# Performance work log

Hardware: AMD Instinct MI355X
Metric: run time of the kernel (lower is better)

The kernel has to match this reference:

```python
import jax, jax.numpy as jnp
import numpy as np

D = 4      # number of tensor modes (leaves of the HT tree)
N = 8      # input dim per mode  (total input  = 8^4 = 4096)
M = 8      # output dim per mode (total output = 8^4 = 4096)
R = 8      # HT rank
B = 512    # batch size
# preorder index of each internal-node core in the stacked `cores` array
CORE_IDX = {(0, 4): 0, (0, 2): 1, (2, 4): 2}


def _contract(a, a_names, b, b_names):
    """tn.contract_between equivalent: contract all shared named axes."""
    shared = [n for n in a_names if n in b_names]
    ax_a = [a_names.index(n) for n in shared]
    ax_b = [b_names.index(n) for n in shared]
    out = jnp.tensordot(a, b, axes=(ax_a, ax_b))
    names = [n for n in a_names if n not in shared] + [n for n in b_names if n not in shared]
    return out, names


def _fwd(x, names, lo, hi, factors, cores):
    """Faithful translation of HTSubTree.forward / build_network.

    Leaf p: factor (in_p, out_p, parent). Internal (lo,hi): core
    (left=parent(lo,mid), right=parent(mid,hi), parent=parent(lo,hi)).
    Contraction order: left subtree, then core, then right subtree; shared
    (pre-connected) edges are contracted automatically, exactly as in
    tn.contract_between on the pre-wired network.
    """
    if hi - lo == 1:
        p = lo
        f_names = [f"in_{p}", f"out_{p}", f"pr_{p}_{p + 1}"]
        return _contract(x, names, factors[p], f_names)
    mid = (lo + hi) // 2
    x, names = _fwd(x, names, lo, mid, factors, cores)
    c_names = [f"pr_{lo}_{mid}", f"pr_{mid}_{hi}", f"pr_{lo}_{hi}"]
    x, names = _contract(x, names, cores[CORE_IDX[(lo, hi)]], c_names)
    return _fwd(x, names, mid, hi, factors, cores)


def setup_inputs() -> dict:
    key = jax.random.key(0)
    k1, k2, k3 = jax.random.split(key, 3)
    x = jax.random.normal(k1, (B, N, N, N, N), dtype=jnp.float32)
    # xavier_normal(fan_in=[in], fan_out=[out, rank]) for factors
    std_f = (2.0 / (N + M * R)) ** 0.5
    factors = jax.random.normal(k2, (D, N, M, R), dtype=jnp.float32) * std_f
    # cores: xavier over rank axes
    std_c = (2.0 / (R + R * R)) ** 0.5
    cores = jax.random.normal(k3, (D - 1, R, R, R), dtype=jnp.float32) * std_c
    return {"x": x, "factors": factors, "cores": cores}


def reference(x, factors, cores):
    names = ["batch"] + [f"in_{p}" for p in range(D)]
    out, names = _fwd(x, names, 0, D, factors, cores)
    # dangling edges: batch, out_0..out_{D-1}, root parent rank -> canonical order
    order = ["batch"] + [f"out_{p}" for p in range(D)] + [f"pr_0_{D}"]
    perm = [names.index(n) for n in order]
    return jnp.transpose(out, perm)  # (B, m0, m1, m2, m3, R)
```

## Files before the change

### kernel.cpp

```cpp
#include <hip/hip_runtime.h>

typedef __attribute__((ext_vector_type(8))) short bf16x8;
typedef __attribute__((ext_vector_type(4))) float f32x4;

static __device__ __forceinline__ short f2bf(float f) {
    union { float f; unsigned u; } v; v.f = f;
    unsigned r = v.u + 0x7fffu + ((v.u >> 16) & 1u);
    return (short)(r >> 16);
}

__global__ __launch_bounds__(256) void ht_pre(const float* __restrict__ factors,
                                              const float* __restrict__ cores,
                                              short* __restrict__ TLTF,
                                              short* __restrict__ VTF) {
    const int bid = blockIdx.x, t = threadIdx.x;
    if (bid < 64) {
        __shared__ float TRl[64][9];
        const int m23 = bid;
        const int m2 = m23 >> 3, m3 = m23 & 7;
        {
            const int v = t * 2;
            const int n23 = v >> 3;
            const int r24 = v & 7;
            const int n2 = n23 >> 3, n3 = n23 & 7;
            const float* f2p = factors + 1024 + n2 * 64 + m2 * 8;
            const float* f3p = factors + 1536 + n3 * 64 + m3 * 8;
            const float* c2p = cores + 1024;
            float s0 = 0.f, s1 = 0.f;
            #pragma unroll
            for (int r23 = 0; r23 < 8; ++r23) {
                float a = f2p[r23];
                #pragma unroll
                for (int r34 = 0; r34 < 8; ++r34) {
                    float wv = a * f3p[r34];
                    s0 += wv * c2p[r23 * 64 + r34 * 8 + r24];
                    s1 += wv * c2p[r23 * 64 + r34 * 8 + r24 + 1];
                }
            }
            TRl[n23][r24] = s0;
            TRl[n23][r24 + 1] = s1;
        }
        __syncthreads();
        {
            const int r = t >> 5, seg = t & 31;
            const int k2b = seg * 16;
            const int r02 = k2b >> 6;
            float c0v[8];
            #pragma unroll
            for (int r24 = 0; r24 < 8; ++r24)
                c0v[r24] = cores[r02 * 64 + r24 * 8 + r];
            short ov[16];
            #pragma unroll
            for (int j = 0; j < 16; ++j) {
                const int n23 = (k2b + j) & 63;
                float s = 0.f;
                #pragma unroll
                for (int r24 = 0; r24 < 8; ++r24)
                    s += TRl[n23][r24] * c0v[r24];
                ov[j] = f2bf(s);
            }
            const int c = m23 * 8 + r;
            const int ct16 = c >> 4, lrow = c & 15;
            const int kb = k2b >> 5;
            const int hi0 = (k2b >> 3) & 3;
            const int base = (ct16 * 16 + kb) * 512 + lrow * 8;
            *(bf16x8*)&VTF[base + hi0 * 128]       = *(bf16x8*)&ov[0];
            *(bf16x8*)&VTF[base + (hi0 + 1) * 128] = *(bf16x8*)&ov[8];
        }
    } else {
        const int idx = ((bid - 64) * 256 + t) * 2;
        const int p = idx >> 6, n01 = idx & 63;
        const int n0 = n01 >> 3, n1 = n01 & 7;
        const int mm = p >> 3, r02 = p & 7;
        const int m0 = mm >> 3, m1 = mm & 7;
        const float* f0 = factors + n0 * 64 + m0 * 8;
        const float* f1a = factors + 512 + n1 * 64 + m1 * 8;
        const float* f1b = f1a + 64;
        const float* c1 = cores + 512;
        float s0 = 0.f, s1 = 0.f;
        #pragma unroll
        for (int r01 = 0; r01 < 8; ++r01) {
            float a = f0[r01];
            #pragma unroll
            for (int r12 = 0; r12 < 8; ++r12) {
                float cv = c1[r01 * 64 + r12 * 8 + r02];
                s0 += a * f1a[r12] * cv;
                s1 += a * f1b[r12] * cv;
            }
        }
        unsigned w0 = (unsigned short)f2bf(s0);
        unsigned w1 = (unsigned short)f2bf(s1);
        const int p16 = p >> 4, prow = p & 15;
        const int half = n01 >> 5, hi = (n01 >> 3) & 3, e = n01 & 7;
        *(unsigned*)&TLTF[(p16 * 2 + half) * 512 + (hi * 16 + prow) * 8 + e] = w0 | (w1 << 16);
    }
}

__global__ __launch_bounds__(256, 2) void ht_main(const float* __restrict__ x,
                                                  const short* __restrict__ TLTF,
                                                  const short* __restrict__ VTF,
                                                  float* __restrict__ out) {
    __shared__ short XT[64 * 64];
    __shared__ short YF[64 * 512];

    const int t = threadIdx.x;
    const int b = blockIdx.x;
    const int w = t >> 6, l = t & 63;
    const int lr = l & 15, lk = l >> 4;

    {
        const float* xb = x + b * 4096;
        #pragma unroll
        for (int j = 0; j < 4; ++j) {
            f32x4 v = *(const f32x4*)(xb + j * 1024 + t * 4);
            int n01 = j * 16 + (t >> 4);
            int rbase = (t & 15) * 4;
            #pragma unroll
            for (int e = 0; e < 4; ++e) {
                int rr = rbase + e;
                XT[rr * 64 + (n01 ^ ((rr & 7) << 3))] = f2bf(v[e]);
            }
        }
    }
    __syncthreads();

    {
        bf16x8 bx[4][2];
        #pragma unroll
        for (int ct = 0; ct < 4; ++ct) {
            int rr = ct * 16 + lr;
            #pragma unroll
            for (int kh = 0; kh < 2; ++kh)
                bx[ct][kh] = *(const bf16x8*)&XT[rr * 64 + (((kh * 4 + lk) ^ (rr & 7))) * 8];
        }
        #pragma unroll
        for (int pt = 0; pt < 8; ++pt) {
            const short* ap = TLTF + (w * 8 + pt) * 1024 + l * 8;
            bf16x8 a0 = *(const bf16x8*)ap;
            bf16x8 a1 = *(const bf16x8*)(ap + 512);
            #pragma unroll
            for (int ct = 0; ct < 4; ++ct) {
                f32x4 d = {0.f, 0.f, 0.f, 0.f};
                d = __builtin_amdgcn_mfma_f32_16x16x32_bf16(a0, bx[ct][0], d, 0, 0, 0);
                d = __builtin_amdgcn_mfma_f32_16x16x32_bf16(a1, bx[ct][1], d, 0, 0, 0);
                #pragma unroll
                for (int reg = 0; reg < 4; ++reg) {
                    int pl = lk * 4 + reg;
                    int m_lo = pt * 2 + (pl >> 3);
                    int k2 = (pl & 7) * 64 + ct * 16 + lr;
                    int kb = k2 >> 5, hi = (k2 >> 3) & 3, e = k2 & 7;
                    YF[(w * 16 + kb) * 512 + (hi * 16 + m_lo) * 8 + e] = f2bf(d[reg]);
                }
            }
        }
    }
    __syncthreads();

    {
        f32x4 acc[4][8];
        #pragma unroll
        for (int rt = 0; rt < 4; ++rt)
            #pragma unroll
            for (int ctl = 0; ctl < 8; ++ctl)
                acc[rt][ctl] = (f32x4){0.f, 0.f, 0.f, 0.f};

        bf16x8 afA[4], afB[4], bvA[8], bvB[8];

        #define LDA(kb, af_)  { _Pragma("unroll") \
            for (int rt = 0; rt < 4; ++rt) \
                af_[rt] = *(const bf16x8*)&YF[(rt * 16 + (kb)) * 512 + l * 8]; }
        #define LDB(kb, bv_)  { _Pragma("unroll") \
            for (int ctl = 0; ctl < 8; ++ctl) \
                bv_[ctl] = *(const bf16x8*)&VTF[((w * 8 + ctl) * 16 + (kb)) * 512 + l * 8]; }
        #define MM(af_, bv_)  { _Pragma("unroll") \
            for (int rt = 0; rt < 4; ++rt) { _Pragma("unroll") \
                for (int ctl = 0; ctl < 8; ++ctl) \
                    acc[rt][ctl] = __builtin_amdgcn_mfma_f32_16x16x32_bf16(af_[rt], bv_[ctl], acc[rt][ctl], 0, 0, 0); } }

        LDA(0, afA); LDB(0, bvA);
        #pragma unroll
        for (int kp = 0; kp < 8; ++kp) {
            LDA(kp * 2 + 1, afB); LDB(kp * 2 + 1, bvB);
            MM(afA, bvA);
            if (kp < 7) { LDA(kp * 2 + 2, afA); LDB(kp * 2 + 2, bvA); }
            MM(afB, bvB);
        }
        #undef LDA
        #undef LDB
        #undef MM

        float* ob = out + b * 32768 + w * 128;
        #pragma unroll
        for (int rt = 0; rt < 4; ++rt)
            #pragma unroll
            for (int ctl = 0; ctl < 8; ++ctl)
                #pragma unroll
                for (int reg = 0; reg < 4; ++reg)
                    ob[(rt * 16 + lk * 4 + reg) * 512 + ctl * 16 + lr] = acc[rt][ctl][reg];
    }
}

extern "C" void kernel_launch(void* const* d_in, const int* in_sizes, int n_in,
                              void* d_out, int out_size, void* d_ws, size_t ws_size,
                              hipStream_t stream) {
    const float* x       = (const float*)d_in[0];
    const float* factors = (const float*)d_in[1];
    const float* cores   = (const float*)d_in[2];
    float* out = (float*)d_out;

    short* TLTF = (short*)d_ws;
    short* VTF  = TLTF + 32768;

    hipLaunchKernelGGL(ht_pre, dim3(128), dim3(256), 0, stream, factors, cores, TLTF, VTF);
    hipLaunchKernelGGL(ht_main, dim3(512), dim3(256), 0, stream, x, TLTF, VTF, out);
}
```

Measured before the change: 125.9 us.

## Use 8 waves per block with swizzled row-major intermediate LDS layout

Doubles ht_main to 512 threads, so each wave owns half as many output column tiles and half the P-rows in stage one. The intermediate Y is now stored row-major in LDS with an XOR swizzle and packed 8-byte writes, replacing the scattered 2-byte stores. The VTF k-ordering in ht_pre changes to match. The explicit double-buffered load pipeline in the main GEMM is dropped in favour of a simple per-kb loop. This trades fewer registers per thread and more parallelism for the loss of manual prefetch.

```diff
diff --git a/kernel.cpp b/kernel.cpp
--- a/kernel.cpp
+++ b/kernel.cpp
@@ -2,6 +2,8 @@
 
 typedef __attribute__((ext_vector_type(8))) short bf16x8;
 typedef __attribute__((ext_vector_type(4))) float f32x4;
+
+struct u32x2 { unsigned x, y; };
 
 static __device__ __forceinline__ short f2bf(float f) {
     union { float f; unsigned u; } v; v.f = f;
@@ -43,26 +45,21 @@
         __syncthreads();
         {
             const int r = t >> 5, seg = t & 31;
-            const int k2b = seg * 16;
-            const int r02 = k2b >> 6;
-            float c0v[8];
-            #pragma unroll
-            for (int r24 = 0; r24 < 8; ++r24)
-                c0v[r24] = cores[r02 * 64 + r24 * 8 + r];
             short ov[16];
             #pragma unroll
             for (int j = 0; j < 16; ++j) {
-                const int n23 = (k2b + j) & 63;
+                const int n23 = seg * 2 + (j >> 3);
+                const int r02 = j & 7;
                 float s = 0.f;
                 #pragma unroll
                 for (int r24 = 0; r24 < 8; ++r24)
-                    s += TRl[n23][r24] * c0v[r24];
+                    s += TRl[n23][r24] * cores[r02 * 64 + r24 * 8 + r];
                 ov[j] = f2bf(s);
             }
             const int c = m23 * 8 + r;
             const int ct16 = c >> 4, lrow = c & 15;
-            const int kb = k2b >> 5;
-            const int hi0 = (k2b >> 3) & 3;
+            const int kb = seg >> 1;
+            const int hi0 = (seg * 2) & 3;
             const int base = (ct16 * 16 + kb) * 512 + lrow * 8;
             *(bf16x8*)&VTF[base + hi0 * 128]       = *(bf16x8*)&ov[0];
             *(bf16x8*)&VTF[base + (hi0 + 1) * 128] = *(bf16x8*)&ov[8];
@@ -96,12 +93,12 @@
     }
 }
 
-__global__ __launch_bounds__(256, 2) void ht_main(const float* __restrict__ x,
+__global__ __launch_bounds__(512, 2) void ht_main(const float* __restrict__ x,
                                                   const short* __restrict__ TLTF,
                                                   const short* __restrict__ VTF,
                                                   float* __restrict__ out) {
     __shared__ short XT[64 * 64];
-    __shared__ short YF[64 * 512];
+    __shared__ short YS[64 * 512];
 
     const int t = threadIdx.x;
     const int b = blockIdx.x;
@@ -111,9 +108,9 @@
     {
         const float* xb = x + b * 4096;
         #pragma unroll
-        for (int j = 0; j < 4; ++j) {
-            f32x4 v = *(const f32x4*)(xb + j * 1024 + t * 4);
-            int n01 = j * 16 + (t >> 4);
+        for (int j = 0; j < 2; ++j) {
+            f32x4 v = *(const f32x4*)(xb + j * 2048 + t * 4);
+            int n01 = j * 32 + (t >> 4);
             int rbase = (t & 15) * 4;
             #pragma unroll
             for (int e = 0; e < 4; ++e) {
@@ -131,69 +128,61 @@
             int rr = ct * 16 + lr;
             #pragma unroll
             for (int kh = 0; kh < 2; ++kh)
-                bx[ct][kh] = *(const bf16x8*)&XT[rr * 64 + (((kh * 4 + lk) ^ (rr & 7))) * 8];
-        }
-        #pragma unroll
-        for (int pt = 0; pt < 8; ++pt) {
-            const short* ap = TLTF + (w * 8 + pt) * 1024 + l * 8;
+                bx[ct][kh] = *(const bf16x8*)&XT[rr * 64 + ((kh * 4 + lk) ^ (rr & 7)) * 8];
+        }
+        #pragma unroll
+        for (int pt = 0; pt < 4; ++pt) {
+            const short* ap = TLTF + (w * 4 + pt) * 1024 + l * 8;
             bf16x8 a0 = *(const bf16x8*)ap;
             bf16x8 a1 = *(const bf16x8*)(ap + 512);
+            const int row = w * 8 + pt * 2 + (lk >> 1);
             #pragma unroll
             for (int ct = 0; ct < 4; ++ct) {
                 f32x4 d = {0.f, 0.f, 0.f, 0.f};
                 d = __builtin_amdgcn_mfma_f32_16x16x32_bf16(a0, bx[ct][0], d, 0, 0, 0);
                 d = __builtin_amdgcn_mfma_f32_16x16x32_bf16(a1, bx[ct][1], d, 0, 0, 0);
-                #pragma unroll
-                for (int reg = 0; reg < 4; ++reg) {
-                    int pl = lk * 4 + reg;
-                    int m_lo = pt * 2 + (pl >> 3);
-                    int k2 = (pl & 7) * 64 + ct * 16 + lr;
-                    int kb = k2 >> 5, hi = (k2 >> 3) & 3, e = k2 & 7;
-                    YF[(w * 16 + kb) * 512 + (hi * 16 + m_lo) * 8 + e] = f2bf(d[reg]);
-                }
+                const int n23 = ct * 16 + lr;
+                unsigned lo = (unsigned short)f2bf(d[0]) | ((unsigned)(unsigned short)f2bf(d[1]) << 16);
+                unsigned hi = (unsigned short)f2bf(d[2]) | ((unsigned)(unsigned short)f2bf(d[3]) << 16);
+                u32x2 val; val.x = lo; val.y = hi;
+                *(u32x2*)&YS[row * 512 + (n23 ^ (row & 7)) * 8 + (lk & 1) * 4] = val;
             }
         }
     }
     __syncthreads();
 
     {
-        f32x4 acc[4][8];
+        f32x4 acc[4][4];
         #pragma unroll
         for (int rt = 0; rt < 4; ++rt)
             #pragma unroll
-            for (int ctl = 0; ctl < 8; ++ctl)
+            for (int ctl = 0; ctl < 4; ++ctl)
                 acc[rt][ctl] = (f32x4){0.f, 0.f, 0.f, 0.f};
 
-        bf16x8 afA[4], afB[4], bvA[8], bvB[8];
-
-        #define LDA(kb, af_)  { _Pragma("unroll") \
-            for (int rt = 0; rt < 4; ++rt) \
-                af_[rt] = *(const bf16x8*)&YF[(rt * 16 + (kb)) * 512 + l * 8]; }
-        #define LDB(kb, bv_)  { _Pragma("unroll") \
-            for (int ctl = 0; ctl < 8; ++ctl) \
-                bv_[ctl] = *(const bf16x8*)&VTF[((w * 8 + ctl) * 16 + (kb)) * 512 + l * 8]; }
-        #define MM(af_, bv_)  { _Pragma("unroll") \
-            for (int rt = 0; rt < 4; ++rt) { _Pragma("unroll") \
-                for (int ctl = 0; ctl < 8; ++ctl) \
-                    acc[rt][ctl] = __builtin_amdgcn_mfma_f32_16x16x32_bf16(af_[rt], bv_[ctl], acc[rt][ctl], 0, 0, 0); } }
-
-        LDA(0, afA); LDB(0, bvA);
-        #pragma unroll
-        for (int kp = 0; kp < 8; ++kp) {
-            LDA(kp * 2 + 1, afB); LDB(kp * 2 + 1, bvB);
-            MM(afA, bvA);
-            if (kp < 7) { LDA(kp * 2 + 2, afA); LDB(kp * 2 + 2, bvA); }
-            MM(afB, bvB);
-        }
-        #undef LDA
-        #undef LDB
-        #undef MM
-
-        float* ob = out + b * 32768 + w * 128;
+        #pragma unroll
+        for (int kb = 0; kb < 16; ++kb) {
+            bf16x8 bv[4];
+            #pragma unroll
+            for (int ctl = 0; ctl < 4; ++ctl)
+                bv[ctl] = *(const bf16x8*)&VTF[((w * 4 + ctl) * 16 + kb) * 512 + l * 8];
+            bf16x8 af[4];
+            #pragma unroll
+            for (int rt = 0; rt < 4; ++rt) {
+                const int row = rt * 16 + lr;
+                af[rt] = *(const bf16x8*)&YS[row * 512 + ((kb * 4 + lk) ^ (lr & 7)) * 8];
+            }
+            #pragma unroll
+            for (int rt = 0; rt < 4; ++rt)
+                #pragma unroll
+                for (int ctl = 0; ctl < 4; ++ctl)
+                    acc[rt][ctl] = __builtin_amdgcn_mfma_f32_16x16x32_bf16(af[rt], bv[ctl], acc[rt][ctl], 0, 0, 0);
+        }
+
+        float* ob = out + b * 32768 + w * 64;
         #pragma unroll
         for (int rt = 0; rt < 4; ++rt)
             #pragma unroll
-            for (int ctl = 0; ctl < 8; ++ctl)
+            for (int ctl = 0; ctl < 4; ++ctl)
                 #pragma unroll
                 for (int reg = 0; reg < 4; ++reg)
                     ob[(rt * 16 + lk * 4 + reg) * 512 + ctl * 16 + lr] = acc[rt][ctl][reg];
@@ -212,5 +201,5 @@
     short* VTF  = TLTF + 32768;
 
     hipLaunchKernelGGL(ht_pre, dim3(128), dim3(256), 0, stream, factors, cores, TLTF, VTF);
-    hipLaunchKernelGGL(ht_main, dim3(512), dim3(256), 0, stream, x, TLTF, VTF, out);
-}
+    hipLaunchKernelGGL(ht_main, dim3(512), dim3(512), 0, stream, x, TLTF, VTF, out);
+}
```

Result: faster. 102.4 us (-18.7%).
